# Kernel optimization log

Measured on AMD Instinct MI355X. Metric: run time of the kernel, lower is better.

Reference implementation:

```python
import jax, jax.numpy as jnp
import numpy as np

N_NODES = 50000
N_EDGES = 800000
D_IN = 128
D_OUT = 128


def setup_inputs() -> dict:
    key = jax.random.key(0)
    k1, k2, k3, k4, k5, k6 = jax.random.split(key, 6)
    stdv = 1.0 / np.sqrt(D_OUT)
    x = jax.random.normal(k1, (N_NODES, D_IN), dtype=jnp.float32)
    weight = jax.random.uniform(k2, (D_IN, D_OUT), dtype=jnp.float32, minval=-stdv, maxval=stdv)
    bias = jax.random.uniform(k3, (D_OUT,), dtype=jnp.float32, minval=-stdv, maxval=stdv)
    edge_weight = jax.random.uniform(k4, (N_EDGES,), dtype=jnp.float32)
    edge_row = jax.random.randint(k5, (N_EDGES,), 0, N_NODES, dtype=jnp.int64)
    edge_col = jax.random.randint(k6, (N_EDGES,), 0, N_NODES, dtype=jnp.int64)
    return {"x": x, "weight": weight, "bias": bias,
            "edge_weight": edge_weight, "edge_row": edge_row, "edge_col": edge_col}


def reference(x, weight, bias, edge_weight, edge_row, edge_col):
    # support = input @ W   -> [N, D_OUT]
    support = x @ weight
    # spmm(adj, support): out[i] = sum over edges (i<-j) of a_ij * support[j]
    gathered = support[edge_col] * edge_weight[:, None]  # [E, D_OUT]
    out = jax.ops.segment_sum(gathered, edge_row, num_segments=N_NODES)
    return out + bias
```

## Files before the change

### kernel.cpp

```cpp
#include <hip/hip_runtime.h>
#include <hip/hip_bf16.h>

#define NN 50000
#define NE 800000
#define D 128

#define RPB 50
#define NB 1000
#define NBP 1024
#define CAP 1024
#define TILE 4096
#define NBIN 196
#define AROWS 64
#define TSTR 136

#define CASTB 1563
#define PACKB 4

#define XH_OFF   0
#define WF_OFF   3200000
#define CUR_OFF  3208192
#define REC_OFF  3209216

typedef short bf16x8 __attribute__((ext_vector_type(8)));
typedef float f32x4 __attribute__((ext_vector_type(4)));

__device__ inline unsigned short f2bf_u(float f) {
    __hip_bfloat16 h = __float2bfloat16(f);
    return __builtin_bit_cast(unsigned short, h);
}
__device__ inline unsigned pack2(float a, float b) {
    return (unsigned)f2bf_u(a) | ((unsigned)f2bf_u(b) << 16);
}
__device__ inline void acc8(float* acc, uint4 v, float w) {
    unsigned dw[4] = {v.x, v.y, v.z, v.w};
    #pragma unroll
    for (int i = 0; i < 4; ++i) {
        float lo = __int_as_float((int)(dw[i] << 16));
        float hi = __int_as_float((int)(dw[i] & 0xffff0000u));
        acc[2 * i]     += w * lo;
        acc[2 * i + 1] += w * hi;
    }
}

__global__ __launch_bounds__(512) void cast_bin_kernel(
    const float* __restrict__ x, const float* __restrict__ W,
    const int* __restrict__ erow, const int* __restrict__ ecol,
    const float* __restrict__ ew,
    unsigned* __restrict__ x_h4, unsigned short* __restrict__ Wf,
    int* __restrict__ cursor, int2* __restrict__ recs)
{
    __shared__ int  lhist[NBP];
    __shared__ int  lexcl[NBP];
    __shared__ int  lbase[NBP];
    __shared__ int  lpair[512];
    __shared__ int2 stag[TILE];

    int b = blockIdx.x;
    int t = threadIdx.x;

    if (b < CASTB) {
        int idx = b * 512 + t;
        if (idx < 800000) {
            const float4* x4 = (const float4*)x;
            float4 v0 = x4[idx * 2];
            float4 v1 = x4[idx * 2 + 1];
            uint4 o;
            o.x = pack2(v0.x, v0.y);
            o.y = pack2(v0.z, v0.w);
            o.z = pack2(v1.x, v1.y);
            o.w = pack2(v1.z, v1.w);
            ((uint4*)x_h4)[idx] = o;
        }
        return;
    }
    if (b < CASTB + PACKB) {
        int flat = (b - CASTB) * 512 + t;
        int lane = flat & 63;
        int c    = (flat >> 6) & 3;
        int nt   = flat >> 8;
        int col  = nt * 16 + (lane & 15);
        int kb   = c * 32 + (lane >> 4) * 8;
        unsigned d[4];
        #pragma unroll
        for (int jj = 0; jj < 4; ++jj) {
            float a  = W[(kb + 2 * jj) * D + col];
            float bb = W[(kb + 2 * jj + 1) * D + col];
            d[jj] = pack2(a, bb);
        }
        uint4 o; o.x = d[0]; o.y = d[1]; o.z = d[2]; o.w = d[3];
        ((uint4*)Wf)[flat] = o;
        return;
    }

    int base = (b - CASTB - PACKB) * TILE;
    int cnt = NE - base; if (cnt > TILE) cnt = TILE;

    lhist[t] = 0;
    lhist[t + 512] = 0;
    __syncthreads();

    int4 r[2], c[2]; float4 w[2]; bool val[2];
    #pragma unroll
    for (int g = 0; g < 2; ++g) {
        int i4 = (base >> 2) + t + g * 512;
        val[g] = (i4 * 4) < NE && (i4 * 4) < (base + TILE);
        if (val[g]) {
            r[g] = ((const int4*)erow)[i4];
            c[g] = ((const int4*)ecol)[i4];
            w[g] = ((const float4*)ew)[i4];
        }
    }
    #pragma unroll
    for (int g = 0; g < 2; ++g) {
        if (val[g]) {
            atomicAdd(&lhist[(unsigned)r[g].x / RPB], 1);
            atomicAdd(&lhist[(unsigned)r[g].y / RPB], 1);
            atomicAdd(&lhist[(unsigned)r[g].z / RPB], 1);
            atomicAdd(&lhist[(unsigned)r[g].w / RPB], 1);
        }
    }
    __syncthreads();

    int a0 = lhist[2 * t], a1 = lhist[2 * t + 1];
    lpair[t] = a0 + a1;
    __syncthreads();
    for (int off = 1; off < 512; off <<= 1) {
        int v = (t >= off) ? lpair[t - off] : 0;
        __syncthreads();
        lpair[t] += v;
        __syncthreads();
    }
    int exclp = lpair[t] - (a0 + a1);
    lexcl[2 * t]     = exclp;
    lexcl[2 * t + 1] = exclp + a0;
    lbase[2 * t]     = a0 ? atomicAdd(&cursor[2 * t], a0) : 0;
    lbase[2 * t + 1] = a1 ? atomicAdd(&cursor[2 * t + 1], a1) : 0;
    lhist[2 * t]     = exclp;
    lhist[2 * t + 1] = exclp + a0;
    __syncthreads();

    #pragma unroll
    for (int g = 0; g < 2; ++g) {
        if (val[g]) {
            int rr[4] = {r[g].x, r[g].y, r[g].z, r[g].w};
            int cc[4] = {c[g].x, c[g].y, c[g].z, c[g].w};
            float wwv[4] = {w[g].x, w[g].y, w[g].z, w[g].w};
            #pragma unroll
            for (int j = 0; j < 4; ++j) {
                int bk = (unsigned)rr[j] / RPB;
                int rank = atomicAdd(&lhist[bk], 1);
                int2 rec;
                rec.x = (rr[j] << 16) | cc[j];
                rec.y = __float_as_int(wwv[j]);
                stag[rank] = rec;
            }
        }
    }
    __syncthreads();

    #pragma unroll
    for (int k = 0; k < 8; ++k) {
        int i = t + k * 512;
        if (i < cnt) {
            int2 rec = stag[i];
            int bk = (((unsigned)rec.x) >> 16) / RPB;
            int pos = lbase[bk] + (i - lexcl[bk]);
            if (pos < CAP)
                recs[(size_t)bk * CAP + pos] = rec;
        }
    }
}

__global__ __launch_bounds__(512) void gat_gemm_kernel(
    const unsigned short* __restrict__ x_h, const int2* __restrict__ recs,
    const int* __restrict__ cursor, const unsigned short* __restrict__ Wf,
    const float* __restrict__ bias, float* __restrict__ out)
{
    __shared__ int2 srec[CAP];
    __shared__ __align__(16) unsigned short tile[AROWS * TSTR];
    __shared__ int rowstart[RPB + 1];
    __shared__ int rowcur[64];
    __shared__ int stmp[64];

    int t = threadIdx.x;
    int b = blockIdx.x;
    int cnt = cursor[b];
    if (cnt > CAP) cnt = CAP;
    int rb = b * RPB;
    const int2* my = recs + (size_t)b * CAP;

    if (t < 64) rowcur[t] = 0;
    __syncthreads();

    int2 r0, r1;
    bool v0 = t < cnt, v1 = t + 512 < cnt;
    if (v0) r0 = my[t];
    if (v1) r1 = my[t + 512];

    if (v0) atomicAdd(&rowcur[(((unsigned)r0.x) >> 16) - rb], 1);
    if (v1) atomicAdd(&rowcur[(((unsigned)r1.x) >> 16) - rb], 1);
    __syncthreads();

    int myc = 0;
    if (t < 64) { myc = rowcur[t]; stmp[t] = myc; }
    __syncthreads();
    for (int off = 1; off < 64; off <<= 1) {
        int v = 0;
        if (t < 64 && t >= off) v = stmp[t - off];
        __syncthreads();
        if (t < 64) stmp[t] += v;
        __syncthreads();
    }
    if (t < 64) { int ex = stmp[t] - myc; if (t <= RPB) rowstart[t] = ex; rowcur[t] = ex; }
    if (t == 0) rowstart[RPB] = cnt;
    __syncthreads();

    if (v0) srec[atomicAdd(&rowcur[(((unsigned)r0.x) >> 16) - rb], 1)] = r0;
    if (v1) srec[atomicAdd(&rowcur[(((unsigned)r1.x) >> 16) - rb], 1)] = r1;
    __syncthreads();

    int q = t & 15;
    int grp = t >> 4;
    const uint4* xv = (const uint4*)x_h;
    #pragma unroll
    for (int it = 0; it < 2; ++it) {
        int rl = it * 32 + grp;
        if (rl < RPB) {
            int p = rowstart[rl], p1 = rowstart[rl + 1];
            float acc[8] = {};
            for (; p + 4 <= p1; p += 4) {
                int2 e0 = srec[p];
                int2 e1 = srec[p + 1];
                int2 e2 = srec[p + 2];
                int2 e3 = srec[p + 3];
                uint4 w0 = xv[(size_t)(e0.x & 0xffff) * 16 + q];
                uint4 w1 = xv[(size_t)(e1.x & 0xffff) * 16 + q];
                uint4 w2 = xv[(size_t)(e2.x & 0xffff) * 16 + q];
                uint4 w3 = xv[(size_t)(e3.x & 0xffff) * 16 + q];
                acc8(acc, w0, __int_as_float(e0.y));
                acc8(acc, w1, __int_as_float(e1.y));
                acc8(acc, w2, __int_as_float(e2.y));
                acc8(acc, w3, __int_as_float(e3.y));
            }
            for (; p < p1; ++p) {
                int2 e = srec[p];
                uint4 w = xv[(size_t)(e.x & 0xffff) * 16 + q];
                acc8(acc, w, __int_as_float(e.y));
            }
            uint4 o;
            o.x = pack2(acc[0], acc[1]);
            o.y = pack2(acc[2], acc[3]);
            o.z = pack2(acc[4], acc[5]);
            o.w = pack2(acc[6], acc[7]);
            *(uint4*)&tile[rl * TSTR + q * 8] = o;
        }
    }
    __syncthreads();

    int wave = t >> 6, lane = t & 63;
    int m = lane & 15, quad = lane >> 4;
    const bf16x8* bp = (const bf16x8*)Wf;
    bf16x8 bfr[4];
    #pragma unroll
    for (int c = 0; c < 4; ++c) bfr[c] = bp[(wave * 4 + c) * 64 + lane];
    float bcol = bias[wave * 16 + m];

    #pragma unroll
    for (int mt = 0; mt < 4; ++mt) {
        f32x4 acc = {0.f, 0.f, 0.f, 0.f};
        #pragma unroll
        for (int c = 0; c < 4; ++c) {
            bf16x8 afr = *(const bf16x8*)&tile[(mt * 16 + m) * TSTR + c * 32 + quad * 8];
            acc = __builtin_amdgcn_mfma_f32_16x16x32_bf16(afr, bfr[c], acc, 0, 0, 0);
        }
        #pragma unroll
        for (int r = 0; r < 4; ++r) {
            int lr = mt * 16 + quad * 4 + r;
            int grow = rb + lr;
            if (lr < RPB && grow < NN)
                out[(size_t)grow * D + wave * 16 + m] = acc[r] + bcol;
        }
    }
}

extern "C" void kernel_launch(void* const* d_in, const int* in_sizes, int n_in,
                              void* d_out, int out_size, void* d_ws, size_t ws_size,
                              hipStream_t stream) {
    const float* x    = (const float*)d_in[0];
    const float* W    = (const float*)d_in[1];
    const float* bias = (const float*)d_in[2];
    const float* ew   = (const float*)d_in[3];
    const int*   erow = (const int*)d_in[4];
    const int*   ecol = (const int*)d_in[5];
    float* out = (float*)d_out;

    unsigned* ws_u = (unsigned*)d_ws;
    unsigned*        x_h4   = ws_u + XH_OFF;
    unsigned short*  x_h    = (unsigned short*)x_h4;
    unsigned short*  Wf     = (unsigned short*)(ws_u + WF_OFF);
    int*             cursor = (int*)(ws_u + CUR_OFF);
    int2*            recs   = (int2*)(ws_u + REC_OFF);

    hipMemsetAsync(cursor, 0, NBP * sizeof(int), stream);
    cast_bin_kernel<<<CASTB + PACKB + NBIN, 512, 0, stream>>>(
        x, W, erow, ecol, ew, x_h4, Wf, cursor, recs);
    gat_gemm_kernel<<<NB, 512, 0, stream>>>(x_h, recs, cursor, Wf, bias, out);
}
```

Measured before the change: 129.8 us.

## Use wave-shuffle scans, smaller binning tiles, interleaved two-row gather loop

Replaces the barrier-heavy LDS prefix scans in both kernels with wavefront __shfl_up scans plus a small cross-wave combine, removing many __syncthreads. Halves the binning tile to 2048 edges so each thread handles one int4 group and twice as many bin blocks run. The gather loop now interleaves rows A and B, two edges each per step, to keep more independent global loads in flight. The trade-off is more global cursor atomics from the extra blocks and more register pressure in the gather.

```diff
diff --git a/kernel.cpp b/kernel.cpp
--- a/kernel.cpp
+++ b/kernel.cpp
@@ -7,10 +7,9 @@
 
 #define RPB 50
 #define NB 1000
-#define NBP 1024
 #define CAP 1024
-#define TILE 4096
-#define NBIN 196
+#define TILE 2048
+#define NBIN 391
 #define AROWS 64
 #define TSTR 136
 
@@ -50,10 +49,11 @@
     unsigned* __restrict__ x_h4, unsigned short* __restrict__ Wf,
     int* __restrict__ cursor, int2* __restrict__ recs)
 {
-    __shared__ int  lhist[NBP];
-    __shared__ int  lexcl[NBP];
-    __shared__ int  lbase[NBP];
-    __shared__ int  lpair[512];
+    __shared__ int  lhist[1024];
+    __shared__ int  lexcl[1024];
+    __shared__ int  lbase[1024];
+    __shared__ int  wsum[8];
+    __shared__ int  wexcl[8];
     __shared__ int2 stag[TILE];
 
     int b = blockIdx.x;
@@ -100,67 +100,63 @@
     lhist[t + 512] = 0;
     __syncthreads();
 
-    int4 r[2], c[2]; float4 w[2]; bool val[2];
-    #pragma unroll
-    for (int g = 0; g < 2; ++g) {
-        int i4 = (base >> 2) + t + g * 512;
-        val[g] = (i4 * 4) < NE && (i4 * 4) < (base + TILE);
-        if (val[g]) {
-            r[g] = ((const int4*)erow)[i4];
-            c[g] = ((const int4*)ecol)[i4];
-            w[g] = ((const float4*)ew)[i4];
-        }
-    }
-    #pragma unroll
-    for (int g = 0; g < 2; ++g) {
-        if (val[g]) {
-            atomicAdd(&lhist[(unsigned)r[g].x / RPB], 1);
-            atomicAdd(&lhist[(unsigned)r[g].y / RPB], 1);
-            atomicAdd(&lhist[(unsigned)r[g].z / RPB], 1);
-            atomicAdd(&lhist[(unsigned)r[g].w / RPB], 1);
-        }
+    int4 r, c; float4 w;
+    int i4 = (base >> 2) + t;
+    bool val = (i4 * 4) < NE;
+    if (val) {
+        r = ((const int4*)erow)[i4];
+        c = ((const int4*)ecol)[i4];
+        w = ((const float4*)ew)[i4];
+        atomicAdd(&lhist[(unsigned)r.x / RPB], 1);
+        atomicAdd(&lhist[(unsigned)r.y / RPB], 1);
+        atomicAdd(&lhist[(unsigned)r.z / RPB], 1);
+        atomicAdd(&lhist[(unsigned)r.w / RPB], 1);
     }
     __syncthreads();
 
     int a0 = lhist[2 * t], a1 = lhist[2 * t + 1];
-    lpair[t] = a0 + a1;
-    __syncthreads();
-    for (int off = 1; off < 512; off <<= 1) {
-        int v = (t >= off) ? lpair[t - off] : 0;
-        __syncthreads();
-        lpair[t] += v;
-        __syncthreads();
-    }
-    int exclp = lpair[t] - (a0 + a1);
-    lexcl[2 * t]     = exclp;
-    lexcl[2 * t + 1] = exclp + a0;
+    int s = a0 + a1;
+    int lane = t & 63, wv = t >> 6;
+    #pragma unroll
+    for (int off = 1; off < 64; off <<= 1) {
+        int v = __shfl_up(s, off, 64);
+        if (lane >= off) s += v;
+    }
+    if (lane == 63) wsum[wv] = s;
+    __syncthreads();
+    if (t < 8) {
+        int e = 0;
+        for (int i = 0; i < t; ++i) e += wsum[i];
+        wexcl[t] = e;
+    }
+    __syncthreads();
+    int exclT = s + wexcl[wv] - (a0 + a1);
+    lexcl[2 * t]     = exclT;
+    lexcl[2 * t + 1] = exclT + a0;
     lbase[2 * t]     = a0 ? atomicAdd(&cursor[2 * t], a0) : 0;
     lbase[2 * t + 1] = a1 ? atomicAdd(&cursor[2 * t + 1], a1) : 0;
-    lhist[2 * t]     = exclp;
-    lhist[2 * t + 1] = exclp + a0;
-    __syncthreads();
-
-    #pragma unroll
-    for (int g = 0; g < 2; ++g) {
-        if (val[g]) {
-            int rr[4] = {r[g].x, r[g].y, r[g].z, r[g].w};
-            int cc[4] = {c[g].x, c[g].y, c[g].z, c[g].w};
-            float wwv[4] = {w[g].x, w[g].y, w[g].z, w[g].w};
-            #pragma unroll
-            for (int j = 0; j < 4; ++j) {
-                int bk = (unsigned)rr[j] / RPB;
-                int rank = atomicAdd(&lhist[bk], 1);
-                int2 rec;
-                rec.x = (rr[j] << 16) | cc[j];
-                rec.y = __float_as_int(wwv[j]);
-                stag[rank] = rec;
-            }
-        }
-    }
-    __syncthreads();
-
-    #pragma unroll
-    for (int k = 0; k < 8; ++k) {
+    lhist[2 * t]     = exclT;
+    lhist[2 * t + 1] = exclT + a0;
+    __syncthreads();
+
+    if (val) {
+        int rr[4] = {r.x, r.y, r.z, r.w};
+        int cc[4] = {c.x, c.y, c.z, c.w};
+        float wwv[4] = {w.x, w.y, w.z, w.w};
+        #pragma unroll
+        for (int j = 0; j < 4; ++j) {
+            int bk = (unsigned)rr[j] / RPB;
+            int rank = atomicAdd(&lhist[bk], 1);
+            int2 rec;
+            rec.x = (rr[j] << 16) | cc[j];
+            rec.y = __float_as_int(wwv[j]);
+            stag[rank] = rec;
+        }
+    }
+    __syncthreads();
+
+    #pragma unroll
+    for (int k = 0; k < 4; ++k) {
         int i = t + k * 512;
         if (i < cnt) {
             int2 rec = stag[i];
@@ -179,9 +175,8 @@
 {
     __shared__ int2 srec[CAP];
     __shared__ __align__(16) unsigned short tile[AROWS * TSTR];
-    __shared__ int rowstart[RPB + 1];
+    __shared__ int rowstart[64];
     __shared__ int rowcur[64];
-    __shared__ int stmp[64];
 
     int t = threadIdx.x;
     int b = blockIdx.x;
@@ -197,23 +192,22 @@
     bool v0 = t < cnt, v1 = t + 512 < cnt;
     if (v0) r0 = my[t];
     if (v1) r1 = my[t + 512];
-
     if (v0) atomicAdd(&rowcur[(((unsigned)r0.x) >> 16) - rb], 1);
     if (v1) atomicAdd(&rowcur[(((unsigned)r1.x) >> 16) - rb], 1);
     __syncthreads();
 
-    int myc = 0;
-    if (t < 64) { myc = rowcur[t]; stmp[t] = myc; }
-    __syncthreads();
-    for (int off = 1; off < 64; off <<= 1) {
-        int v = 0;
-        if (t < 64 && t >= off) v = stmp[t - off];
-        __syncthreads();
-        if (t < 64) stmp[t] += v;
-        __syncthreads();
-    }
-    if (t < 64) { int ex = stmp[t] - myc; if (t <= RPB) rowstart[t] = ex; rowcur[t] = ex; }
-    if (t == 0) rowstart[RPB] = cnt;
+    if (t < 64) {
+        int cth = rowcur[t];
+        int s = cth;
+        #pragma unroll
+        for (int off = 1; off < 64; off <<= 1) {
+            int v = __shfl_up(s, off, 64);
+            if (t >= off) s += v;
+        }
+        int ex = s - cth;
+        rowstart[t] = ex;
+        rowcur[t] = ex;
+    }
     __syncthreads();
 
     if (v0) srec[atomicAdd(&rowcur[(((unsigned)r0.x) >> 16) - rb], 1)] = r0;
@@ -222,38 +216,75 @@
 
     int q = t & 15;
     int grp = t >> 4;
+    int rlA = grp;
+    int rlB = 32 + grp;
     const uint4* xv = (const uint4*)x_h;
-    #pragma unroll
-    for (int it = 0; it < 2; ++it) {
-        int rl = it * 32 + grp;
-        if (rl < RPB) {
-            int p = rowstart[rl], p1 = rowstart[rl + 1];
-            float acc[8] = {};
-            for (; p + 4 <= p1; p += 4) {
-                int2 e0 = srec[p];
-                int2 e1 = srec[p + 1];
-                int2 e2 = srec[p + 2];
-                int2 e3 = srec[p + 3];
-                uint4 w0 = xv[(size_t)(e0.x & 0xffff) * 16 + q];
-                uint4 w1 = xv[(size_t)(e1.x & 0xffff) * 16 + q];
-                uint4 w2 = xv[(size_t)(e2.x & 0xffff) * 16 + q];
-                uint4 w3 = xv[(size_t)(e3.x & 0xffff) * 16 + q];
-                acc8(acc, w0, __int_as_float(e0.y));
-                acc8(acc, w1, __int_as_float(e1.y));
-                acc8(acc, w2, __int_as_float(e2.y));
-                acc8(acc, w3, __int_as_float(e3.y));
-            }
-            for (; p < p1; ++p) {
-                int2 e = srec[p];
-                uint4 w = xv[(size_t)(e.x & 0xffff) * 16 + q];
-                acc8(acc, w, __int_as_float(e.y));
-            }
-            uint4 o;
-            o.x = pack2(acc[0], acc[1]);
-            o.y = pack2(acc[2], acc[3]);
-            o.z = pack2(acc[4], acc[5]);
-            o.w = pack2(acc[6], acc[7]);
-            *(uint4*)&tile[rl * TSTR + q * 8] = o;
+
+    int pA = rowstart[rlA], eA = rowstart[rlA + 1];
+    int pB = 0, eB = 0;
+    bool hasB = (rlB < RPB);
+    if (hasB) { pB = rowstart[rlB]; eB = rowstart[rlB + 1]; }
+
+    float accA[8] = {}, accB[8] = {};
+    while (pA + 2 <= eA && pB + 2 <= eB) {
+        int2 ea0 = srec[pA], ea1 = srec[pA + 1];
+        int2 eb0 = srec[pB], eb1 = srec[pB + 1];
+        uint4 va0 = xv[(size_t)(ea0.x & 0xffff) * 16 + q];
+        uint4 va1 = xv[(size_t)(ea1.x & 0xffff) * 16 + q];
+        uint4 vb0 = xv[(size_t)(eb0.x & 0xffff) * 16 + q];
+        uint4 vb1 = xv[(size_t)(eb1.x & 0xffff) * 16 + q];
+        acc8(accA, va0, __int_as_float(ea0.y));
+        acc8(accA, va1, __int_as_float(ea1.y));
+        acc8(accB, vb0, __int_as_float(eb0.y));
+        acc8(accB, vb1, __int_as_float(eb1.y));
+        pA += 2; pB += 2;
+    }
+    for (; pA + 4 <= eA; pA += 4) {
+        int2 e0 = srec[pA], e1 = srec[pA + 1], e2 = srec[pA + 2], e3 = srec[pA + 3];
+        uint4 w0 = xv[(size_t)(e0.x & 0xffff) * 16 + q];
+        uint4 w1 = xv[(size_t)(e1.x & 0xffff) * 16 + q];
+        uint4 w2 = xv[(size_t)(e2.x & 0xffff) * 16 + q];
+        uint4 w3 = xv[(size_t)(e3.x & 0xffff) * 16 + q];
+        acc8(accA, w0, __int_as_float(e0.y));
+        acc8(accA, w1, __int_as_float(e1.y));
+        acc8(accA, w2, __int_as_float(e2.y));
+        acc8(accA, w3, __int_as_float(e3.y));
+    }
+    for (; pA < eA; ++pA) {
+        int2 e = srec[pA];
+        uint4 w = xv[(size_t)(e.x & 0xffff) * 16 + q];
+        acc8(accA, w, __int_as_float(e.y));
+    }
+    for (; pB + 4 <= eB; pB += 4) {
+        int2 e0 = srec[pB], e1 = srec[pB + 1], e2 = srec[pB + 2], e3 = srec[pB + 3];
+        uint4 w0 = xv[(size_t)(e0.x & 0xffff) * 16 + q];
+        uint4 w1 = xv[(size_t)(e1.x & 0xffff) * 16 + q];
+        uint4 w2 = xv[(size_t)(e2.x & 0xffff) * 16 + q];
+        uint4 w3 = xv[(size_t)(e3.x & 0xffff) * 16 + q];
+        acc8(accB, w0, __int_as_float(e0.y));
+        acc8(accB, w1, __int_as_float(e1.y));
+        acc8(accB, w2, __int_as_float(e2.y));
+        acc8(accB, w3, __int_as_float(e3.y));
+    }
+    for (; pB < eB; ++pB) {
+        int2 e = srec[pB];
+        uint4 w = xv[(size_t)(e.x & 0xffff) * 16 + q];
+        acc8(accB, w, __int_as_float(e.y));
+    }
+    {
+        uint4 o;
+        o.x = pack2(accA[0], accA[1]);
+        o.y = pack2(accA[2], accA[3]);
+        o.z = pack2(accA[4], accA[5]);
+        o.w = pack2(accA[6], accA[7]);
+        *(uint4*)&tile[rlA * TSTR + q * 8] = o;
+        if (hasB) {
+            uint4 p;
+            p.x = pack2(accB[0], accB[1]);
+            p.y = pack2(accB[2], accB[3]);
+            p.z = pack2(accB[4], accB[5]);
+            p.w = pack2(accB[6], accB[7]);
+            *(uint4*)&tile[rlB * TSTR + q * 8] = p;
         }
     }
     __syncthreads();
@@ -302,7 +333,7 @@
     int*             cursor = (int*)(ws_u + CUR_OFF);
     int2*            recs   = (int2*)(ws_u + REC_OFF);
 
-    hipMemsetAsync(cursor, 0, NBP * sizeof(int), stream);
+    hipMemsetAsync(cursor, 0, 1024 * sizeof(int), stream);
     cast_bin_kernel<<<CASTB + PACKB + NBIN, 512, 0, stream>>>(
         x, W, erow, ecol, ew, x_h4, Wf, cursor, recs);
     gat_gemm_kernel<<<NB, 512, 0, stream>>>(x_h, recs, cursor, Wf, bias, out);
```

New measurement: 145.7 us. 1.12x slower.
